# Performance work log

Hardware: AMD Instinct MI355X
Metric: run time of the kernel (lower is better)

The kernel has to match this reference:

```python
import jax, jax.numpy as jnp
import numpy as np

EPS = 1e-5


def _ln(x, g, b):
    mu = jnp.mean(x, axis=-1, keepdims=True)
    var = jnp.var(x, axis=-1, keepdims=True)
    return (x - mu) * jax.lax.rsqrt(var + EPS) * g + b


def setup_inputs() -> dict:
    key = jax.random.key(0)
    ks = jax.random.split(key, 24)
    B, S, SD, PD, AD = 2, 512, 512, 128, 64
    H = PD * 2
    s = 0.02
    inp = {
        "sequence_input": jax.random.normal(ks[0], (B, S, SD), jnp.float32),
        "pair_input": jax.random.normal(ks[1], (B, S // 2, S // 2, PD), jnp.float32),
        # SequenceToPairBlock params
        "sn_g": jnp.ones((SD,), jnp.float32),
        "sn_b": jnp.zeros((SD,), jnp.float32),
        "Wq": jax.random.normal(ks[2], (SD, PD), jnp.float32) * s,
        "Wk": jax.random.normal(ks[3], (SD, PD), jnp.float32) * s,
        "Wyq": jax.random.normal(ks[4], (SD, PD), jnp.float32) * s,
        "Wyk": jax.random.normal(ks[5], (SD, PD), jnp.float32) * s,
        "Wdist": jax.random.normal(ks[6], (3, PD), jnp.float32) * s,
        "Wout": jax.random.normal(ks[7], (PD, PD), jnp.float32) * s,
        "bout": jnp.zeros((PD,), jnp.float32),
        # RowAttentionBlock params
        "rn_g": jnp.ones((PD,), jnp.float32),
        "rn_b": jnp.zeros((PD,), jnp.float32),
        "Wrq": jax.random.normal(ks[8], (PD, AD), jnp.float32) * s,
        "Wrk": jax.random.normal(ks[9], (PD, AD), jnp.float32) * s,
        "Wrv": jax.random.normal(ks[10], (PD, AD), jnp.float32) * s,
        "brv": jnp.zeros((AD,), jnp.float32),
        "Wro": jax.random.normal(ks[11], (AD, PD), jnp.float32) * s,
        "bro": jnp.zeros((PD,), jnp.float32),
        # PairMLPBlock params
        "mn_g": jnp.ones((PD,), jnp.float32),
        "mn_b": jnp.zeros((PD,), jnp.float32),
        "W1": jax.random.normal(ks[12], (PD, H), jnp.float32) * s,
        "b1": jnp.zeros((H,), jnp.float32),
        "W2": jax.random.normal(ks[13], (H, PD), jnp.float32) * s,
        "b2": jnp.zeros((PD,), jnp.float32),
    }
    return inp


def reference(sequence_input, pair_input, sn_g, sn_b, Wq, Wk, Wyq, Wyk, Wdist, Wout, bout,
              rn_g, rn_b, Wrq, Wrk, Wrv, brv, Wro, bro, mn_g, mn_b, W1, b1, W2, b2):
    # ---- SequenceToPairBlock ----
    x = _ln(sequence_input, sn_g, sn_b)               # [B,S,SD]
    B, S, SD = x.shape
    x = x.reshape(B, S // 2, 2, SD).mean(axis=2)       # avg_pool1d k=2,s=2 (S even) -> [B,P,SD]
    P = x.shape[1]
    q = x @ Wq                                         # [B,P,PD]
    k = x @ Wk
    pair_qk = q[:, :, None, :] + k[:, None, :, :]      # [B,P,P,PD]
    idx = jnp.arange(P, dtype=x.dtype)
    dist = idx[:, None] - idx[None, :]
    dist_scale = jnp.abs(dist) / max(1.0, float(P - 1))
    dist_feats = jnp.stack([dist_scale, jnp.sign(dist), jnp.exp(-dist_scale)], axis=-1)  # [P,P,3]
    pair_dist = dist_feats @ Wdist                     # [P,P,PD], broadcast over batch
    gx = jax.nn.gelu(x, approximate=False)
    yq = gx @ Wyq
    yk = gx @ Wyk
    pair_outer = yq[:, :, None, :] + yk[:, None, :, :]
    y = (pair_qk + pair_dist[None] + pair_outer) @ Wout + bout  # [B,P,P,PD]

    x = pair_input + y

    # ---- RowAttentionBlock (dropout off / eval) ----
    yn = _ln(x, rn_g, rn_b)
    qa = yn @ Wrq                                      # [B,P,P,AD]
    ka = yn @ Wrk
    va = yn @ Wrv + brv
    scale = 1.0 / jnp.sqrt(jnp.asarray(qa.shape[-1], x.dtype))
    logits = jnp.einsum('bird,bisd->birs', qa, ka) * scale
    attn = jax.nn.softmax(logits, axis=-1)
    o = jnp.einsum('birs,bisd->bird', attn, va)
    x = x + (o @ Wro + bro)

    # ---- PairMLPBlock ----
    h = _ln(x, mn_g, mn_b)
    x = x + (jax.nn.relu(h @ W1 + b1) @ W2 + b2)
    return x
```

## Files before the change

### kernel.cpp

```cpp
#include <hip/hip_runtime.h>
#include <hip/hip_bf16.h>

using bf16 = __hip_bfloat16;
typedef unsigned int uint;
typedef unsigned short ushort;
typedef __attribute__((ext_vector_type(8))) short bf16x8;
typedef __attribute__((ext_vector_type(4))) float f32x4;


__device__ __forceinline__ float bfraw(uint u) { return __uint_as_float(u << 16); }
__device__ __forceinline__ ushort f2bf(float f) {
    bf16 h = __float2bfloat16(f);
    return *reinterpret_cast<ushort*>(&h);
}
__device__ __forceinline__ float lbf(ushort u) { return __uint_as_float(((uint)u) << 16); }

#define MFMA_B16(a, b, c) __builtin_amdgcn_mfma_f32_16x16x32_bf16((a), (b), (c), 0, 0, 0)

__global__ __launch_bounds__(256) void k_ln_pool(
    const float* __restrict__ seq, const float* __restrict__ g,
    const float* __restrict__ be, float* __restrict__ x2)
{
    __shared__ float red[4][4];
    int bp = blockIdx.x;
    int t  = threadIdx.x;
    const float* r0 = seq + (size_t)(bp * 2) * 512;
    const float* r1 = r0 + 512;

    float a0 = r0[t], a1 = r0[t + 256];
    float c0 = r1[t], c1 = r1[t + 256];

    float s0 = a0 + a1, q0 = a0 * a0 + a1 * a1;
    float s1 = c0 + c1, q1 = c0 * c0 + c1 * c1;
#pragma unroll
    for (int off = 32; off; off >>= 1) {
        s0 += __shfl_xor(s0, off); q0 += __shfl_xor(q0, off);
        s1 += __shfl_xor(s1, off); q1 += __shfl_xor(q1, off);
    }
    int w = t >> 6, l = t & 63;
    if (l == 0) { red[0][w] = s0; red[1][w] = q0; red[2][w] = s1; red[3][w] = q1; }
    __syncthreads();
    s0 = red[0][0] + red[0][1] + red[0][2] + red[0][3];
    q0 = red[1][0] + red[1][1] + red[1][2] + red[1][3];
    s1 = red[2][0] + red[2][1] + red[2][2] + red[2][3];
    q1 = red[3][0] + red[3][1] + red[3][2] + red[3][3];

    const float inv = 1.0f / 512.0f;
    float mu0 = s0 * inv, var0 = q0 * inv - mu0 * mu0, rs0 = rsqrtf(var0 + 1e-5f);
    float mu1 = s1 * inv, var1 = q1 * inv - mu1 * mu1, rs1 = rsqrtf(var1 + 1e-5f);

    float g0 = g[t], g1 = g[t + 256];
    float e0 = be[t], e1 = be[t + 256];

    float o0 = 0.5f * ((a0 - mu0) * rs0 * g0 + e0 + (c0 - mu1) * rs1 * g0 + e0);
    float o1 = 0.5f * ((a1 - mu0) * rs0 * g1 + e1 + (c1 - mu1) * rs1 * g1 + e1);

    float* xo = x2 + (size_t)bp * 512;
    xo[t] = o0; xo[t + 256] = o1;
}

__global__ __launch_bounds__(128) void k_proj(
    const float* __restrict__ x2,
    const float* __restrict__ Wq, const float* __restrict__ Wk,
    const float* __restrict__ Wyq, const float* __restrict__ Wyk,
    const float* __restrict__ Wout, const float* __restrict__ bout,
    float* __restrict__ a2, float* __restrict__ c2)
{
    __shared__ float xr[512], gxr[512], ar[128], cr[128];
    int row = blockIdx.x;
    int t   = threadIdx.x;

    for (int u = t; u < 512; u += 128) {
        float v = x2[(size_t)row * 512 + u];
        xr[u]  = v;
        gxr[u] = 0.5f * v * (1.0f + erff(v * 0.70710678118654752f));
    }
    __syncthreads();

    float a = 0.f, c = 0.f;
    for (int s = 0; s < 512; s++) {
        float xs = xr[s], gs = gxr[s];
        a += xs * Wq[s * 128 + t] + gs * Wyq[s * 128 + t];
        c += xs * Wk[s * 128 + t] + gs * Wyk[s * 128 + t];
    }
    ar[t] = a; cr[t] = c;
    __syncthreads();

    float A = bout[t], C = 0.f;
    for (int u = 0; u < 128; u++) {
        float wv = Wout[u * 128 + t];
        A += ar[u] * wv;
        C += cr[u] * wv;
    }
    a2[(size_t)row * 128 + t] = A;
    c2[(size_t)row * 128 + t] = C;
}

__global__ __launch_bounds__(128) void k_wd2(
    const float* __restrict__ Wdist, const float* __restrict__ Wout,
    float* __restrict__ wd2)
{
    int t = threadIdx.x;
#pragma unroll
    for (int f = 0; f < 3; f++) {
        float acc = 0.f;
        for (int u = 0; u < 128; u++)
            acc += Wdist[f * 128 + u] * Wout[u * 128 + t];
        wd2[f * 128 + t] = acc;
    }
}

__global__ __launch_bounds__(512) void k_wt(
    const float* __restrict__ Wrq, const float* __restrict__ Wrk,
    const float* __restrict__ Wrv, ushort* __restrict__ wqF,
    ushort* __restrict__ wkF, ushort* __restrict__ wvF)
{
    int idx = blockIdx.x * 512 + threadIdx.x;
    int m = idx >> 13;
    int o = idx & 8191;
    int f = o >> 9;
    int l = (o >> 3) & 63;
    int j = o & 7;
    int nt = f >> 2, kf = f & 3;
    const float* W = (m == 0) ? Wrq : (m == 1) ? Wrk : Wrv;
    ushort* T = (m == 0) ? wqF : (m == 1) ? wkF : wvF;
    T[o] = f2bf(W[(32 * kf + 8 * (l >> 4) + j) * 64 + 16 * nt + (l & 15)]);
}

__global__ __launch_bounds__(512) void k_wt12(
    const float* __restrict__ W1, const float* __restrict__ W2,
    ushort* __restrict__ w1F, ushort* __restrict__ w2F)
{
    int idx = blockIdx.x * 512 + threadIdx.x;
    int o = idx & 32767;
    int f = o >> 9;
    int l = (o >> 3) & 63;
    int j = o & 7;
    int kb = f >> 5, nt = (f >> 2) & 7, kf = f & 3;
    if (idx < 32768) {
        int R = 128 * kb + 16 * nt + (l & 15);
        int C = 32 * kf + 8 * (l >> 4) + j;
        w1F[o] = f2bf(W1[C * 256 + R]);
    } else {
        int R2 = 16 * nt + (l & 15);
        int C2 = 128 * kb + 32 * kf + 8 * (l >> 4) + j;
        w2F[o] = f2bf(W2[C2 * 128 + R2]);
    }
}

__global__ __launch_bounds__(256) void k_assemble(
    const float* __restrict__ pair, const float* __restrict__ a2,
    const float* __restrict__ c2, const float* __restrict__ wd2,
    float* __restrict__ xout)
{
    size_t idx = (size_t)blockIdx.x * 256 + threadIdx.x;
    int d = (int)(idx & 127);
    size_t r = idx >> 7;
    int j = (int)(r & 255); r >>= 8;
    int i = (int)(r & 255);
    int b = (int)(r >> 8);

    float ds = fabsf((float)(i - j)) * (1.0f / 255.0f);
    float sg = (float)((i > j) - (i < j));
    float ex = __expf(-ds);

    float v = pair[idx]
            + a2[(size_t)(b * 256 + i) * 128 + d]
            + c2[(size_t)(b * 256 + j) * 128 + d]
            + ds * wd2[d] + sg * wd2[128 + d] + ex * wd2[256 + d];
    xout[idx] = v;
}

__global__ __launch_bounds__(512, 2) void k_attn_mfma(
    float* __restrict__ x,
    const float* __restrict__ rn_g, const float* __restrict__ rn_b,
    const ushort* __restrict__ wqF, const ushort* __restrict__ wkF,
    const ushort* __restrict__ wvF, const float* __restrict__ brv,
    const float* __restrict__ Wro, const float* __restrict__ bro)
{
    __shared__ __align__(16) unsigned char smem[131072];

    int tid = threadIdx.x;
    int w  = tid >> 6;
    int l  = tid & 63;
    int g  = l >> 4;
    int lr = l & 15;
    size_t base = (size_t)blockIdx.x * 32768;

    float gl0 = rn_g[l], gl1 = rn_g[l + 64];
    float el0 = rn_b[l], el1 = rn_b[l + 64];

    for (int h = 0; h < 2; h++) {
        for (int rr = 0; rr < 16; rr++) {
            int rloc = 16 * w + rr;
            size_t ro = base + (size_t)(128 * h + rloc) * 128;
            float x0 = x[ro + l], x1 = x[ro + l + 64];
            float s = x0 + x1, q = x0 * x0 + x1 * x1;
#pragma unroll
            for (int off = 32; off; off >>= 1) { s += __shfl_xor(s, off); q += __shfl_xor(q, off); }
            float mu = s * (1.0f / 128.0f);
            float var = q * (1.0f / 128.0f) - mu * mu;
            float rs = rsqrtf(var + 1e-5f);
            int sw = (rloc & 7) << 4;
            *(ushort*)(smem + 65536 + rloc * 256 + ((2 * l) ^ sw))        = f2bf((x0 - mu) * rs * gl0 + el0);
            *(ushort*)(smem + 65536 + rloc * 256 + ((2 * (l + 64)) ^ sw)) = f2bf((x1 - mu) * rs * gl1 + el1);
        }
        asm volatile("s_waitcnt lgkmcnt(0)" ::: "memory");

        bf16x8 afr[4];
        int arow = 16 * w + lr;
#pragma unroll
        for (int kf = 0; kf < 4; kf++) {
            int ab = 65536 + arow * 256 + ((16 * g + 64 * kf) ^ ((arow & 7) << 4));
            afr[kf] = *(const bf16x8*)(smem + ab);
        }
#pragma unroll
        for (int m = 0; m < 3; m++) {
            const ushort* wT = (m == 0) ? wqF : (m == 1) ? wkF : wvF;
            f32x4 acc[4];
#pragma unroll
            for (int nt = 0; nt < 4; nt++) acc[nt] = (f32x4){0.f, 0.f, 0.f, 0.f};
#pragma unroll
            for (int kf = 0; kf < 4; kf++) {
#pragma unroll
                for (int nt = 0; nt < 4; nt++) {
                    bf16x8 bfr = *(const bf16x8*)(wT + (((nt << 2) | kf) << 9) + (l << 3));
                    acc[nt] = MFMA_B16(afr[kf], bfr, acc[nt]);
                }
            }
#pragma unroll
            for (int nt = 0; nt < 4; nt++) {
                int col = lr + 16 * nt;
                float bv = (m == 2) ? brv[col] : 0.f;
#pragma unroll
                for (int i = 0; i < 4; i++) {
                    int qrow = 128 * h + 16 * w + 4 * g + i;
                    float v = acc[nt][i];
                    if (m == 0) {
                        int ad = 98304 + qrow * 128 + ((2 * col) ^ ((qrow & 7) << 4));
                        *(ushort*)(smem + ad) = f2bf(v * 0.125f);
                    } else if (m == 1) {
                        int ad = qrow * 128 + ((2 * col) ^ ((qrow & 7) << 4));
                        *(ushort*)(smem + ad) = f2bf(v);
                    } else {
                        int ad = 32768 + col * 512 + ((2 * qrow) ^ ((col & 7) << 4));
                        *(ushort*)(smem + ad) = f2bf(v + bv);
                    }
                }
            }
        }
    }
    __syncthreads();

    bf16x8 qf[2][2];
#pragma unroll
    for (int mt = 0; mt < 2; mt++)
#pragma unroll
        for (int kf = 0; kf < 2; kf++) {
            int qrow = 32 * w + 16 * mt + lr;
            int ab = 98304 + qrow * 128 + ((16 * g + 64 * kf) ^ ((qrow & 7) << 4));
            qf[mt][kf] = *(const bf16x8*)(smem + ab);
        }
    __syncthreads();

    float m_run[2][4], l_run[2][4];
    f32x4 oacc[2][4];
#pragma unroll
    for (int mt = 0; mt < 2; mt++)
#pragma unroll
        for (int i = 0; i < 4; i++) { m_run[mt][i] = -INFINITY; l_run[mt][i] = 0.f; }
#pragma unroll
    for (int mt = 0; mt < 2; mt++)
#pragma unroll
        for (int nt = 0; nt < 4; nt++) oacc[mt][nt] = (f32x4){0.f, 0.f, 0.f, 0.f};

    for (int t = 0; t < 2; t++) {
        f32x4 sacc[2][8];
#pragma unroll
        for (int mt = 0; mt < 2; mt++)
#pragma unroll
            for (int nt = 0; nt < 8; nt++) sacc[mt][nt] = (f32x4){0.f, 0.f, 0.f, 0.f};
#pragma unroll
        for (int nt = 0; nt < 8; nt++) {
#pragma unroll
            for (int kf = 0; kf < 2; kf++) {
                int key = 128 * t + 16 * nt + lr;
                int ab = key * 128 + ((16 * g + 64 * kf) ^ ((key & 7) << 4));
                bf16x8 bfr = *(const bf16x8*)(smem + ab);
#pragma unroll
                for (int mt = 0; mt < 2; mt++)
                    sacc[mt][nt] = MFMA_B16(qf[mt][kf], bfr, sacc[mt][nt]);
            }
        }
#pragma unroll
        for (int mt = 0; mt < 2; mt++) {
#pragma unroll
            for (int i = 0; i < 4; i++) {
                float mx = sacc[mt][0][i];
#pragma unroll
                for (int nt = 1; nt < 8; nt++) mx = fmaxf(mx, sacc[mt][nt][i]);
#pragma unroll
                for (int off = 1; off < 16; off <<= 1) mx = fmaxf(mx, __shfl_xor(mx, off));
                float mnew = fmaxf(m_run[mt][i], mx);
                float corr = __expf(m_run[mt][i] - mnew);
                m_run[mt][i] = mnew;
                int qrow = 32 * w + 16 * mt + 4 * g + i;
                int swq = (qrow & 7) << 4;
                float rs = 0.f;
#pragma unroll
                for (int nt = 0; nt < 8; nt++) {
                    float p = __expf(sacc[mt][nt][i] - mnew);
                    rs += p;
                    int col = lr + 16 * nt;
                    *(ushort*)(smem + 65536 + qrow * 256 + ((2 * col) ^ swq)) = f2bf(p);
                }
#pragma unroll
                for (int off = 1; off < 16; off <<= 1) rs += __shfl_xor(rs, off);
                l_run[mt][i] = l_run[mt][i] * corr + rs;
#pragma unroll
                for (int nt = 0; nt < 4; nt++) oacc[mt][nt][i] *= corr;
            }
        }
        asm volatile("s_waitcnt lgkmcnt(0)" ::: "memory");

#pragma unroll
        for (int kf = 0; kf < 4; kf++) {
            bf16x8 pfr[2];
#pragma unroll
            for (int mt = 0; mt < 2; mt++) {
                int qrow = 32 * w + 16 * mt + lr;
                int ab = 65536 + qrow * 256 + ((16 * g + 64 * kf) ^ ((qrow & 7) << 4));
                pfr[mt] = *(const bf16x8*)(smem + ab);
            }
#pragma unroll
            for (int nt = 0; nt < 4; nt++) {
                int d = lr + 16 * nt;
                int bb = 32768 + d * 512 + ((16 * g + 64 * kf + 256 * t) ^ ((d & 7) << 4));
                bf16x8 bfr = *(const bf16x8*)(smem + bb);
#pragma unroll
                for (int mt = 0; mt < 2; mt++)
                    oacc[mt][nt] = MFMA_B16(pfr[mt], bfr, oacc[mt][nt]);
            }
        }
    }
    __syncthreads();

#pragma unroll
    for (int mt = 0; mt < 2; mt++)
#pragma unroll
        for (int i = 0; i < 4; i++) {
            float rl = 1.0f / l_run[mt][i];
            int qrow = 32 * w + 16 * mt + 4 * g + i;
            int swq = (qrow & 7) << 4;
#pragma unroll
            for (int nt = 0; nt < 4; nt++) {
                int col = lr + 16 * nt;
                *(ushort*)(smem + 65536 + qrow * 128 + ((2 * col) ^ swq)) = f2bf(oacc[mt][nt][i] * rl);
            }
        }
    for (int e = tid; e < 8192; e += 512) {
        int k = e >> 7, c = e & 127;
        int ad = c * 128 + ((2 * k) ^ ((c & 7) << 4));
        *(ushort*)(smem + ad) = f2bf(Wro[e]);
    }
    __syncthreads();

#pragma unroll
    for (int mt = 0; mt < 2; mt++) {
        bf16x8 ofr[2];
#pragma unroll
        for (int kf = 0; kf < 2; kf++) {
            int orow = 32 * w + 16 * mt + lr;
            int ab = 65536 + orow * 128 + ((16 * g + 64 * kf) ^ ((orow & 7) << 4));
            ofr[kf] = *(const bf16x8*)(smem + ab);
        }
#pragma unroll
        for (int nt = 0; nt < 8; nt++) {
            f32x4 acc = (f32x4){0.f, 0.f, 0.f, 0.f};
#pragma unroll
            for (int kf = 0; kf < 2; kf++) {
                int c = lr + 16 * nt;
                int bb = c * 128 + ((16 * g + 64 * kf) ^ ((c & 7) << 4));
                bf16x8 bfr = *(const bf16x8*)(smem + bb);
                acc = MFMA_B16(ofr[kf], bfr, acc);
            }
            int col = lr + 16 * nt;
            float brod = bro[col];
#pragma unroll
            for (int i = 0; i < 4; i++) {
                int qrow = 32 * w + 16 * mt + 4 * g + i;
                size_t off = base + (size_t)qrow * 128 + col;
                x[off] = x[off] + acc[i] + brod;
            }
        }
    }
}

__global__ __launch_bounds__(64, 4) void k_mlp_mfma(
    float* __restrict__ x,
    const float* __restrict__ mn_g, const float* __restrict__ mn_b,
    const ushort* __restrict__ w1F, const ushort* __restrict__ w2F,
    const float* __restrict__ b1, const float* __restrict__ b2)
{
    __shared__ __align__(16) unsigned char smem[5120];
    int l = threadIdx.x;
    int g = l >> 4, lr = l & 15;
    size_t rbase = (size_t)blockIdx.x * 16;

    {
        float gl0 = mn_g[l], gl1 = mn_g[l + 64];
        float el0 = mn_b[l], el1 = mn_b[l + 64];
#pragma unroll
        for (int bb = 0; bb < 4; bb++) {
            float a0[4], a1[4];
#pragma unroll
            for (int rr = 0; rr < 4; rr++) {
                size_t ro = (rbase + 4 * bb + rr) * 128;
                a0[rr] = x[ro + l];
                a1[rr] = x[ro + l + 64];
            }
#pragma unroll
            for (int rr = 0; rr < 4; rr++) {
                int rloc = 4 * bb + rr;
                float x0 = a0[rr], x1 = a1[rr];
                float s = x0 + x1, q = x0 * x0 + x1 * x1;
#pragma unroll
                for (int off = 32; off; off >>= 1) { s += __shfl_xor(s, off); q += __shfl_xor(q, off); }
                float mu = s * (1.0f / 128.0f);
                float var = q * (1.0f / 128.0f) - mu * mu;
                float rs = rsqrtf(var + 1e-5f);
                int sw = (rloc & 7) << 4;
                *(ushort*)(smem + rloc * 256 + ((2 * l) ^ sw))        = f2bf((x0 - mu) * rs * gl0 + el0);
                *(ushort*)(smem + rloc * 256 + ((2 * (l + 64)) ^ sw)) = f2bf((x1 - mu) * rs * gl1 + el1);
            }
        }
    }
    asm volatile("s_waitcnt lgkmcnt(0)" ::: "memory");

    bf16x8 afr[4];
#pragma unroll
    for (int kf = 0; kf < 4; kf++) {
        afr[kf] = *(const bf16x8*)(smem + lr * 256 + ((16 * g + 64 * kf) ^ ((lr & 7) << 4)));
    }

    f32x4 oacc[8];
#pragma unroll
    for (int nt = 0; nt < 8; nt++) oacc[nt] = (f32x4){0.f, 0.f, 0.f, 0.f};

#pragma unroll
    for (int kb = 0; kb < 2; kb++) {
#pragma unroll
        for (int cc = 0; cc < 4; cc++) {
#pragma unroll
            for (int nt2 = 0; nt2 < 2; nt2++) {
                int nt = 2 * cc + nt2;
                f32x4 acc = (f32x4){0.f, 0.f, 0.f, 0.f};
#pragma unroll
                for (int kf = 0; kf < 4; kf++) {
                    bf16x8 bfr = *(const bf16x8*)(w1F + (((((kb << 3) | nt) << 2) | kf) << 9) + (l << 3));
                    acc = MFMA_B16(afr[kf], bfr, acc);
                }
                float bb1 = b1[128 * kb + 16 * nt + lr];
                int colc = lr + 16 * nt2;
#pragma unroll
                for (int i = 0; i < 4; i++) {
                    int row = 4 * g + i;
                    int ad = 4096 + row * 64 + ((2 * colc) ^ ((row & 3) << 4));
                    *(ushort*)(smem + ad) = f2bf(fmaxf(acc[i] + bb1, 0.f));
                }
            }
            asm volatile("s_waitcnt lgkmcnt(0)" ::: "memory");

            bf16x8 hfr = *(const bf16x8*)(smem + 4096 + lr * 64 + ((16 * g) ^ ((lr & 3) << 4)));
#pragma unroll
            for (int nt = 0; nt < 8; nt++) {
                bf16x8 bfr = *(const bf16x8*)(w2F + (((((kb << 3) | nt) << 2) | cc) << 9) + (l << 3));
                oacc[nt] = MFMA_B16(hfr, bfr, oacc[nt]);
            }
            asm volatile("s_waitcnt lgkmcnt(0)" ::: "memory");
        }
    }

#pragma unroll
    for (int nt = 0; nt < 8; nt++) {
        int col = 16 * nt + lr;
#pragma unroll
        for (int i = 0; i < 4; i++) {
            int row = 4 * g + i;
            int ad = row * 256 + ((2 * col) ^ ((row & 7) << 4));
            *(ushort*)(smem + ad) = f2bf(oacc[nt][i]);
        }
    }
    asm volatile("s_waitcnt lgkmcnt(0)" ::: "memory");
    {
        float b20 = b2[l], b21 = b2[l + 64];
#pragma unroll
        for (int rr = 0; rr < 16; rr++) {
            int sw = (rr & 7) << 4;
            float d0 = lbf(*(const ushort*)(smem + rr * 256 + ((2 * l) ^ sw)));
            float d1 = lbf(*(const ushort*)(smem + rr * 256 + ((2 * (l + 64)) ^ sw)));
            size_t ro = (rbase + rr) * 128;
            x[ro + l]      = x[ro + l]      + d0 + b20;
            x[ro + l + 64] = x[ro + l + 64] + d1 + b21;
        }
    }
}

extern "C" void kernel_launch(void* const* d_in, const int* in_sizes, int n_in,
                              void* d_out, int out_size, void* d_ws, size_t ws_size,
                              hipStream_t stream)
{
    const float* seq   = (const float*)d_in[0];
    const float* pair  = (const float*)d_in[1];
    const float* sn_g  = (const float*)d_in[2];
    const float* sn_b  = (const float*)d_in[3];
    const float* Wq    = (const float*)d_in[4];
    const float* Wk    = (const float*)d_in[5];
    const float* Wyq   = (const float*)d_in[6];
    const float* Wyk   = (const float*)d_in[7];
    const float* Wdist = (const float*)d_in[8];
    const float* Wout  = (const float*)d_in[9];
    const float* bout  = (const float*)d_in[10];
    const float* rn_g  = (const float*)d_in[11];
    const float* rn_b  = (const float*)d_in[12];
    const float* Wrq   = (const float*)d_in[13];
    const float* Wrk   = (const float*)d_in[14];
    const float* Wrv   = (const float*)d_in[15];
    const float* brv   = (const float*)d_in[16];
    const float* Wro   = (const float*)d_in[17];
    const float* bro   = (const float*)d_in[18];
    const float* mn_g  = (const float*)d_in[19];
    const float* mn_b  = (const float*)d_in[20];
    const float* W1    = (const float*)d_in[21];
    const float* b1    = (const float*)d_in[22];
    const float* W2    = (const float*)d_in[23];
    const float* b2    = (const float*)d_in[24];
    (void)in_sizes; (void)n_in; (void)out_size; (void)ws_size;

    float*  x2   = (float*)d_ws;
    float*  a2   = x2 + 262144;
    float*  c2   = a2 + 65536;
    float*  wd2  = c2 + 65536;
    ushort* wqF  = (ushort*)(wd2 + 512);
    ushort* wkF  = wqF + 8192;
    ushort* wvF  = wkF + 8192;
    ushort* w1F  = wvF + 8192;
    ushort* w2F  = w1F + 32768;
    float*  xres = (float*)d_out;

    k_ln_pool  <<<512,   256, 0, stream>>>(seq, sn_g, sn_b, x2);
    k_proj     <<<512,   128, 0, stream>>>(x2, Wq, Wk, Wyq, Wyk, Wout, bout, a2, c2);
    k_wd2      <<<1,     128, 0, stream>>>(Wdist, Wout, wd2);
    k_wt       <<<48,    512, 0, stream>>>(Wrq, Wrk, Wrv, wqF, wkF, wvF);
    k_wt12     <<<128,   512, 0, stream>>>(W1, W2, w1F, w2F);
    k_assemble <<<65536, 256, 0, stream>>>(pair, a2, c2, wd2, xres);
    k_attn_mfma<<<512,   512, 0, stream>>>(xres, rn_g, rn_b, wqF, wkF, wvF, brv, Wro, bro);
    k_mlp_mfma <<<8192,  64,  0, stream>>>(xres, mn_g, mn_b, w1F, w2F, b1, b2);
}
```

Baseline: 242.8 us.

## Split row attention into QKV projection and small-block flash attention kernels

Replaces the monolithic 512-thread row-attention kernel with two kernels. The first computes LayerNorm plus Q/K/V projections into pre-swizzled bf16 MFMA fragment buffers in workspace. The second runs flash-style attention per 32-query chunk and applies the output projection with a bf16 MFMA using a pre-swizzled Wro. The aim is more, smaller blocks (4096 single-wave blocks) for better occupancy and an MFMA output projection, at the cost of writing and re-reading about 48 MB of Q/K/V intermediates. The old path remains as a fallback if the workspace is too small.

After: 274.5 us. 13.1% more time.

```diff
diff --git a/kernel.cpp b/kernel.cpp
--- a/kernel.cpp
+++ b/kernel.cpp
@@ -16,6 +16,7 @@
 __device__ __forceinline__ float lbf(ushort u) { return __uint_as_float(((uint)u) << 16); }
 
 #define MFMA_B16(a, b, c) __builtin_amdgcn_mfma_f32_16x16x32_bf16((a), (b), (c), 0, 0, 0)
+#define LGKM0() asm volatile("s_waitcnt lgkmcnt(0)" ::: "memory")
 
 __global__ __launch_bounds__(256) void k_ln_pool(
     const float* __restrict__ seq, const float* __restrict__ g,
@@ -112,8 +113,9 @@
 
 __global__ __launch_bounds__(512) void k_wt(
     const float* __restrict__ Wrq, const float* __restrict__ Wrk,
-    const float* __restrict__ Wrv, ushort* __restrict__ wqF,
-    ushort* __restrict__ wkF, ushort* __restrict__ wvF)
+    const float* __restrict__ Wrv, const float* __restrict__ Wro,
+    ushort* __restrict__ wqF, ushort* __restrict__ wkF,
+    ushort* __restrict__ wvF, ushort* __restrict__ wroF)
 {
     int idx = blockIdx.x * 512 + threadIdx.x;
     int m = idx >> 13;
@@ -121,10 +123,15 @@
     int f = o >> 9;
     int l = (o >> 3) & 63;
     int j = o & 7;
-    int nt = f >> 2, kf = f & 3;
-    const float* W = (m == 0) ? Wrq : (m == 1) ? Wrk : Wrv;
-    ushort* T = (m == 0) ? wqF : (m == 1) ? wkF : wvF;
-    T[o] = f2bf(W[(32 * kf + 8 * (l >> 4) + j) * 64 + 16 * nt + (l & 15)]);
+    if (m < 3) {
+        int nt = f >> 2, kf = f & 3;
+        const float* W = (m == 0) ? Wrq : (m == 1) ? Wrk : Wrv;
+        ushort* T = (m == 0) ? wqF : (m == 1) ? wkF : wvF;
+        T[o] = f2bf(W[(32 * kf + 8 * (l >> 4) + j) * 64 + 16 * nt + (l & 15)]);
+    } else {
+        int nt = f >> 1, kf2 = f & 1;
+        wroF[o] = f2bf(Wro[(32 * kf2 + 8 * (l >> 4) + j) * 128 + 16 * nt + (l & 15)]);
+    }
 }
 
 __global__ __launch_bounds__(512) void k_wt12(
@@ -171,6 +178,256 @@
     xout[idx] = v;
 }
 
+__global__ __launch_bounds__(64, 4) void k_qkv(
+    const float* __restrict__ x,
+    const float* __restrict__ rn_g, const float* __restrict__ rn_b,
+    const ushort* __restrict__ wqF, const ushort* __restrict__ wkF,
+    const ushort* __restrict__ wvF, const float* __restrict__ brv,
+    ushort* __restrict__ qA, ushort* __restrict__ kB, ushort* __restrict__ vB)
+{
+    __shared__ __align__(16) unsigned char smem[12288];
+    int l = threadIdx.x;
+    int g = l >> 4, lr = l & 15;
+    int s = blockIdx.x >> 3;
+    int c = blockIdx.x & 7;
+    size_t xbase = (size_t)s * 32768 + (size_t)(32 * c) * 128;
+
+    {
+        float gl0 = rn_g[l], gl1 = rn_g[l + 64];
+        float el0 = rn_b[l], el1 = rn_b[l + 64];
+#pragma unroll
+        for (int bb = 0; bb < 8; bb++) {
+            float a0[4], a1[4];
+#pragma unroll
+            for (int rr = 0; rr < 4; rr++) {
+                size_t ro = xbase + (size_t)(4 * bb + rr) * 128;
+                a0[rr] = x[ro + l]; a1[rr] = x[ro + l + 64];
+            }
+#pragma unroll
+            for (int rr = 0; rr < 4; rr++) {
+                int rloc = 4 * bb + rr;
+                float x0 = a0[rr], x1 = a1[rr];
+                float sS = x0 + x1, qS = x0 * x0 + x1 * x1;
+#pragma unroll
+                for (int off = 32; off; off >>= 1) { sS += __shfl_xor(sS, off); qS += __shfl_xor(qS, off); }
+                float mu = sS * (1.0f / 128.0f);
+                float var = qS * (1.0f / 128.0f) - mu * mu;
+                float rs = rsqrtf(var + 1e-5f);
+                int sw = (rloc & 7) << 4;
+                *(ushort*)(smem + rloc * 256 + ((2 * l) ^ sw))        = f2bf((x0 - mu) * rs * gl0 + el0);
+                *(ushort*)(smem + rloc * 256 + ((2 * (l + 64)) ^ sw)) = f2bf((x1 - mu) * rs * gl1 + el1);
+            }
+        }
+    }
+    LGKM0();
+
+    bf16x8 afr[2][4];
+#pragma unroll
+    for (int mt = 0; mt < 2; mt++)
+#pragma unroll
+        for (int kf = 0; kf < 4; kf++) {
+            int row = 16 * mt + lr;
+            afr[mt][kf] = *(const bf16x8*)(smem + row * 256 + ((16 * g + 64 * kf) ^ ((row & 7) << 4)));
+        }
+
+    unsigned char* dscr = smem + 8192;
+
+#pragma unroll
+    for (int mqk = 0; mqk < 2; mqk++) {
+        const ushort* wF = mqk ? wkF : wqF;
+        ushort* dst = mqk ? kB : qA;
+        float scale = mqk ? 1.0f : 0.125f;
+#pragma unroll
+        for (int mt = 0; mt < 2; mt++) {
+#pragma unroll
+            for (int nt = 0; nt < 4; nt++) {
+                f32x4 acc = (f32x4){0.f, 0.f, 0.f, 0.f};
+#pragma unroll
+                for (int kf = 0; kf < 4; kf++) {
+                    bf16x8 bfr = *(const bf16x8*)(wF + (((nt << 2) | kf) << 9) + (l << 3));
+                    acc = MFMA_B16(afr[mt][kf], bfr, acc);
+                }
+                int col = lr + 16 * nt;
+#pragma unroll
+                for (int i = 0; i < 4; i++) {
+                    int row = 4 * g + i + 16 * mt;
+                    int ad = row * 128 + ((2 * col) ^ ((row & 7) << 4));
+                    *(ushort*)(dscr + ad) = f2bf(acc[i] * scale);
+                }
+            }
+        }
+        LGKM0();
+#pragma unroll
+        for (int mt = 0; mt < 2; mt++)
+#pragma unroll
+            for (int kf2 = 0; kf2 < 2; kf2++) {
+                int row = 16 * mt + lr;
+                int rd = row * 128 + ((64 * kf2 + 16 * g) ^ ((row & 7) << 4));
+                bf16x8 v = *(const bf16x8*)(dscr + rd);
+                *(bf16x8*)(dst + ((size_t)((s * 16 + 2 * c + mt) * 2 + kf2) << 9) + (l << 3)) = v;
+            }
+        LGKM0();
+    }
+
+#pragma unroll
+    for (int mt = 0; mt < 2; mt++) {
+#pragma unroll
+        for (int nt = 0; nt < 4; nt++) {
+            f32x4 acc = (f32x4){0.f, 0.f, 0.f, 0.f};
+#pragma unroll
+            for (int kf = 0; kf < 4; kf++) {
+                bf16x8 bfr = *(const bf16x8*)(wvF + (((nt << 2) | kf) << 9) + (l << 3));
+                acc = MFMA_B16(afr[mt][kf], bfr, acc);
+            }
+            int d = lr + 16 * nt;
+            float bv = brv[d];
+#pragma unroll
+            for (int i = 0; i < 4; i++) {
+                int kk = 4 * g + i + 16 * mt;
+                int ad = d * 64 + ((2 * kk) ^ ((d & 3) << 4));
+                *(ushort*)(dscr + ad) = f2bf(acc[i] + bv);
+            }
+        }
+    }
+    LGKM0();
+#pragma unroll
+    for (int nt2 = 0; nt2 < 4; nt2++) {
+        int d = 16 * nt2 + lr;
+        int rd = d * 64 + ((16 * g) ^ ((d & 3) << 4));
+        bf16x8 vv = *(const bf16x8*)(dscr + rd);
+        *(bf16x8*)(vB + ((size_t)((s * 4 + nt2) * 8 + c) << 9) + (l << 3)) = vv;
+    }
+}
+
+__global__ __launch_bounds__(64, 2) void k_attn2(
+    float* __restrict__ x,
+    const ushort* __restrict__ qA, const ushort* __restrict__ kB,
+    const ushort* __restrict__ vB, const ushort* __restrict__ wroF,
+    const float* __restrict__ bro)
+{
+    __shared__ __align__(16) unsigned char smem[4096];
+    int l = threadIdx.x, g = l >> 4, lr = l & 15;
+    int s = blockIdx.x >> 3, qc = blockIdx.x & 7;
+
+    bf16x8 qf[2][2];
+#pragma unroll
+    for (int mt = 0; mt < 2; mt++)
+#pragma unroll
+        for (int kf2 = 0; kf2 < 2; kf2++)
+            qf[mt][kf2] = *(const bf16x8*)(qA + ((size_t)((s * 16 + 2 * qc + mt) * 2 + kf2) << 9) + (l << 3));
+
+    float m_run[2][4], l_run[2][4];
+    f32x4 oacc[2][4];
+#pragma unroll
+    for (int mt = 0; mt < 2; mt++)
+#pragma unroll
+        for (int i = 0; i < 4; i++) { m_run[mt][i] = -INFINITY; l_run[mt][i] = 0.f; }
+#pragma unroll
+    for (int mt = 0; mt < 2; mt++)
+#pragma unroll
+        for (int nt = 0; nt < 4; nt++) oacc[mt][nt] = (f32x4){0.f, 0.f, 0.f, 0.f};
+
+    for (int t = 0; t < 2; t++) {
+#pragma unroll
+        for (int mt = 0; mt < 2; mt++) {
+            f32x4 sacc[8];
+#pragma unroll
+            for (int nt = 0; nt < 8; nt++) sacc[nt] = (f32x4){0.f, 0.f, 0.f, 0.f};
+#pragma unroll
+            for (int nt = 0; nt < 8; nt++) {
+                int kt = 8 * t + nt;
+#pragma unroll
+                for (int kf2 = 0; kf2 < 2; kf2++) {
+                    bf16x8 kfr = *(const bf16x8*)(kB + ((size_t)((s * 16 + kt) * 2 + kf2) << 9) + (l << 3));
+                    sacc[nt] = MFMA_B16(qf[mt][kf2], kfr, sacc[nt]);
+                }
+            }
+#pragma unroll
+            for (int i = 0; i < 4; i++) {
+                float mx = sacc[0][i];
+#pragma unroll
+                for (int nt = 1; nt < 8; nt++) mx = fmaxf(mx, sacc[nt][i]);
+#pragma unroll
+                for (int off = 1; off < 16; off <<= 1) mx = fmaxf(mx, __shfl_xor(mx, off));
+                float mnew = fmaxf(m_run[mt][i], mx);
+                float corr = __expf(m_run[mt][i] - mnew);
+                m_run[mt][i] = mnew;
+                int row = 4 * g + i;
+                int swp = (row & 7) << 4;
+                float rs = 0.f;
+#pragma unroll
+                for (int nt = 0; nt < 8; nt++) {
+                    float p = __expf(sacc[nt][i] - mnew);
+                    rs += p;
+                    int key = lr + 16 * nt;
+                    *(ushort*)(smem + row * 256 + ((2 * key) ^ swp)) = f2bf(p);
+                }
+#pragma unroll
+                for (int off = 1; off < 16; off <<= 1) rs += __shfl_xor(rs, off);
+                l_run[mt][i] = l_run[mt][i] * corr + rs;
+#pragma unroll
+                for (int nt = 0; nt < 4; nt++) oacc[mt][nt][i] *= corr;
+            }
+            LGKM0();
+#pragma unroll
+            for (int kc = 0; kc < 4; kc++) {
+                int prow = lr;
+                bf16x8 pfr = *(const bf16x8*)(smem + prow * 256 + ((64 * kc + 16 * g) ^ ((prow & 7) << 4)));
+#pragma unroll
+                for (int nt4 = 0; nt4 < 4; nt4++) {
+                    bf16x8 vfr = *(const bf16x8*)(vB + ((size_t)((s * 4 + nt4) * 8 + 4 * t + kc) << 9) + (l << 3));
+                    oacc[mt][nt4] = MFMA_B16(pfr, vfr, oacc[mt][nt4]);
+                }
+            }
+            LGKM0();
+        }
+    }
+
+#pragma unroll
+    for (int mt = 0; mt < 2; mt++)
+#pragma unroll
+        for (int i = 0; i < 4; i++) {
+            float rl = 1.0f / l_run[mt][i];
+            int row = 4 * g + i + 16 * mt;
+            int swo = (row & 7) << 4;
+#pragma unroll
+            for (int nt = 0; nt < 4; nt++) {
+                int col = lr + 16 * nt;
+                *(ushort*)(smem + row * 128 + ((2 * col) ^ swo)) = f2bf(oacc[mt][nt][i] * rl);
+            }
+        }
+    LGKM0();
+    bf16x8 ofr[2][2];
+#pragma unroll
+    for (int mt = 0; mt < 2; mt++)
+#pragma unroll
+        for (int kf2 = 0; kf2 < 2; kf2++) {
+            int row = 16 * mt + lr;
+            int rd = row * 128 + ((64 * kf2 + 16 * g) ^ ((row & 7) << 4));
+            ofr[mt][kf2] = *(const bf16x8*)(smem + rd);
+        }
+#pragma unroll
+    for (int mt = 0; mt < 2; mt++) {
+#pragma unroll
+        for (int nt = 0; nt < 8; nt++) {
+            f32x4 acc = (f32x4){0.f, 0.f, 0.f, 0.f};
+#pragma unroll
+            for (int kf2 = 0; kf2 < 2; kf2++) {
+                bf16x8 wfr = *(const bf16x8*)(wroF + (((nt << 1) | kf2) << 9) + (l << 3));
+                acc = MFMA_B16(ofr[mt][kf2], wfr, acc);
+            }
+            int col = lr + 16 * nt;
+            float brod = bro[col];
+#pragma unroll
+            for (int i = 0; i < 4; i++) {
+                int row = 32 * qc + 16 * mt + 4 * g + i;
+                size_t off = (size_t)s * 32768 + (size_t)row * 128 + col;
+                x[off] = x[off] + acc[i] + brod;
+            }
+        }
+    }
+}
+
 __global__ __launch_bounds__(512, 2) void k_attn_mfma(
     float* __restrict__ x,
     const float* __restrict__ rn_g, const float* __restrict__ rn_b,
@@ -205,7 +462,7 @@
             *(ushort*)(smem + 65536 + rloc * 256 + ((2 * l) ^ sw))        = f2bf((x0 - mu) * rs * gl0 + el0);
             *(ushort*)(smem + 65536 + rloc * 256 + ((2 * (l + 64)) ^ sw)) = f2bf((x1 - mu) * rs * gl1 + el1);
         }
-        asm volatile("s_waitcnt lgkmcnt(0)" ::: "memory");
+        LGKM0();
 
         bf16x8 afr[4];
         int arow = 16 * w + lr;
@@ -321,7 +578,7 @@
                 for (int nt = 0; nt < 4; nt++) oacc[mt][nt][i] *= corr;
             }
         }
-        asm volatile("s_waitcnt lgkmcnt(0)" ::: "memory");
+        LGKM0();
 
 #pragma unroll
         for (int kf = 0; kf < 4; kf++) {
@@ -435,7 +692,7 @@
             }
         }
     }
-    asm volatile("s_waitcnt lgkmcnt(0)" ::: "memory");
+    LGKM0();
 
     bf16x8 afr[4];
 #pragma unroll
@@ -469,7 +726,7 @@
                     *(ushort*)(smem + ad) = f2bf(fmaxf(acc[i] + bb1, 0.f));
                 }
             }
-            asm volatile("s_waitcnt lgkmcnt(0)" ::: "memory");
+            LGKM0();
 
             bf16x8 hfr = *(const bf16x8*)(smem + 4096 + lr * 64 + ((16 * g) ^ ((lr & 3) << 4)));
 #pragma unroll
@@ -477,7 +734,7 @@
                 bf16x8 bfr = *(const bf16x8*)(w2F + (((((kb << 3) | nt) << 2) | cc) << 9) + (l << 3));
                 oacc[nt] = MFMA_B16(hfr, bfr, oacc[nt]);
             }
-            asm volatile("s_waitcnt lgkmcnt(0)" ::: "memory");
+            LGKM0();
         }
     }
 
@@ -491,7 +748,7 @@
             *(ushort*)(smem + ad) = f2bf(oacc[nt][i]);
         }
     }
-    asm volatile("s_waitcnt lgkmcnt(0)" ::: "memory");
+    LGKM0();
     {
         float b20 = b2[l], b21 = b2[l + 64];
 #pragma unroll
@@ -535,7 +792,7 @@
     const float* b1    = (const float*)d_in[22];
     const float* W2    = (const float*)d_in[23];
     const float* b2    = (const float*)d_in[24];
-    (void)in_sizes; (void)n_in; (void)out_size; (void)ws_size;
+    (void)in_sizes; (void)n_in; (void)out_size;
 
     float*  x2   = (float*)d_ws;
     float*  a2   = x2 + 262144;
@@ -544,16 +801,28 @@
     ushort* wqF  = (ushort*)(wd2 + 512);
     ushort* wkF  = wqF + 8192;
     ushort* wvF  = wkF + 8192;
-    ushort* w1F  = wvF + 8192;
+    ushort* wroF = wvF + 8192;
+    ushort* w1F  = wroF + 8192;
     ushort* w2F  = w1F + 32768;
+    ushort* qA   = w2F + 32768;
+    ushort* kBp  = qA + 8388608;
+    ushort* vBp  = kBp + 8388608;
     float*  xres = (float*)d_out;
+
+    const size_t WS_NEED_SPLIT = 52103168ull;
+    bool use_split = (ws_size >= WS_NEED_SPLIT);
 
     k_ln_pool  <<<512,   256, 0, stream>>>(seq, sn_g, sn_b, x2);
     k_proj     <<<512,   128, 0, stream>>>(x2, Wq, Wk, Wyq, Wyk, Wout, bout, a2, c2);
     k_wd2      <<<1,     128, 0, stream>>>(Wdist, Wout, wd2);
-    k_wt       <<<48,    512, 0, stream>>>(Wrq, Wrk, Wrv, wqF, wkF, wvF);
+    k_wt       <<<64,    512, 0, stream>>>(Wrq, Wrk, Wrv, Wro, wqF, wkF, wvF, wroF);
     k_wt12     <<<128,   512, 0, stream>>>(W1, W2, w1F, w2F);
     k_assemble <<<65536, 256, 0, stream>>>(pair, a2, c2, wd2, xres);
-    k_attn_mfma<<<512,   512, 0, stream>>>(xres, rn_g, rn_b, wqF, wkF, wvF, brv, Wro, bro);
+    if (use_split) {
+        k_qkv  <<<4096,  64,  0, stream>>>(xres, rn_g, rn_b, wqF, wkF, wvF, brv, qA, kBp, vBp);
+        k_attn2<<<4096,  64,  0, stream>>>(xres, qA, kBp, vBp, wroF, bro);
+    } else {
+        k_attn_mfma<<<512, 512, 0, stream>>>(xres, rn_g, rn_b, wqF, wkF, wvF, brv, Wro, bro);
+    }
     k_mlp_mfma <<<8192,  64,  0, stream>>>(xres, mn_g, mn_b, w1F, w2F, b1, b2);
 }
```
